# Optimization experiments

Measured on AMD Instinct MI355X. Metric: run time of the kernel, lower is better.

The kernel has to match this reference:

```python
import jax, jax.numpy as jnp
import numpy as np

EPS = 1e-7
MAX_TAN_NORM = 10.0  # safe_expmap0 clamp


def logmap0(x):
    # x: [..., D] Lorentz point, x[..., 0] = time component (>= 1)
    x0 = x[..., :1]
    xs = x[..., 1:]
    d = jnp.arccosh(jnp.clip(x0, 1.0 + EPS, None))          # geodesic distance to origin
    ns = jnp.clip(jnp.linalg.norm(xs, axis=-1, keepdims=True), EPS, None)
    return jnp.concatenate([jnp.zeros_like(x0), d * xs / ns], axis=-1)


def safe_expmap0(u):
    # u: tangent at origin; time component is projected out (proju at origin)
    us = u[..., 1:]
    n = jnp.clip(jnp.linalg.norm(us, axis=-1, keepdims=True), EPS, None)
    nc = jnp.minimum(n, MAX_TAN_NORM)                        # clamp norm for stability
    usc = us * (nc / n)
    return jnp.concatenate([jnp.cosh(nc), jnp.sinh(nc) * usc / nc], axis=-1)


def projx(x):
    # re-project onto the hyperboloid: x0 = sqrt(1 + ||xs||^2)
    xs = x[..., 1:]
    x0 = jnp.sqrt(1.0 + jnp.sum(xs * xs, axis=-1, keepdims=True))
    return jnp.concatenate([x0, xs], axis=-1)


def lorentz_linear(x_hyp, W, b):
    t = logmap0(x_hyp)
    y = t @ W.T + b
    return projx(safe_expmap0(y))


def setup_inputs() -> dict:
    key = jax.random.key(0)
    ks = jax.random.split(key, 8)
    N, D_IN, D_HID, D_OUT = 8192, 1024, 4096, 1024
    s = 0.02
    x_sp = jax.random.normal(ks[0], (N, D_IN), dtype=jnp.float32)
    x_hyp = projx(x_sp)  # valid Lorentz point (time comp overwritten)
    W1 = jax.random.normal(ks[1], (D_HID, D_IN), dtype=jnp.float32) * s
    b1 = jnp.zeros((D_HID,), dtype=jnp.float32)
    W2 = jax.random.normal(ks[2], (D_HID, D_HID), dtype=jnp.float32) * s
    b2 = jnp.zeros((D_HID,), dtype=jnp.float32)
    W3 = jax.random.normal(ks[3], (D_OUT, D_HID), dtype=jnp.float32) * s
    b3 = jnp.zeros((D_OUT,), dtype=jnp.float32)
    return {"x_hyp": x_hyp, "W1": W1, "b1": b1, "W2": W2, "b2": b2, "W3": W3, "b3": b3}


def reference(x_hyp, W1, b1, W2, b2, W3, b3):
    # layers[:-1] with inter-layer logmap0 -> (dropout=identity in eval) -> expmap0 -> projx
    h = lorentz_linear(x_hyp, W1, b1)
    h = projx(safe_expmap0(logmap0(h)))
    h = lorentz_linear(h, W2, b2)
    h = projx(safe_expmap0(logmap0(h)))
    return lorentz_linear(h, W3, b3)
```

## Files before the change

kernel.cpp:

```cpp
#include <hip/hip_runtime.h>
#include <stdint.h>

#define EPSF 1e-7f
#define MAXTAN 10.0f

typedef __bf16 bf16x8 __attribute__((ext_vector_type(8)));
typedef float floatx4 __attribute__((ext_vector_type(4)));
typedef __attribute__((address_space(3))) void lds_void_t;
typedef __attribute__((address_space(1))) void gbl_void_t;

__device__ __forceinline__ unsigned short f2bf(float x) {
  union { float f; uint32_t u; } v; v.f = x;
  uint32_t u = v.u;
  u += 0x7fffu + ((u >> 16) & 1u);
  return (unsigned short)(u >> 16);
}
__device__ __forceinline__ float bf2f(unsigned short h) {
  union { uint32_t u; float f; } v; v.u = ((uint32_t)h) << 16;
  return v.f;
}

__global__ void k_sniff(const unsigned short* __restrict__ x, int* __restrict__ mode) {
  if (threadIdx.x == 0 && blockIdx.x == 0) {
    int sane = 0;
    for (int i = 0; i < 128; ++i) {
      unsigned short h = x[i];
      int e = (h >> 7) & 0xFF;
      if ((h & 0x7FFF) == 0 || (e >= 96 && e <= 140)) ++sane;
    }
    *mode = (sane >= 120) ? 1 : 0;
  }
}

__global__ void k_prep(const void* __restrict__ xv, unsigned short* __restrict__ xb,
                       float* __restrict__ sc0, float* __restrict__ x0c,
                       const int* __restrict__ mode) {
  const int row = blockIdx.x;
  const int tid = threadIdx.x;
  float4 v;
  if (*mode) {
    ushort4 u = ((const ushort4*)((const unsigned short*)xv + (size_t)row * 1024))[tid];
    v.x = bf2f(u.x); v.y = bf2f(u.y); v.z = bf2f(u.z); v.w = bf2f(u.w);
  } else {
    v = ((const float4*)((const float*)xv + (size_t)row * 1024))[tid];
  }
  ushort4 o;
  o.x = f2bf(v.x); o.y = f2bf(v.y); o.z = f2bf(v.z); o.w = f2bf(v.w);
  ((ushort4*)(xb + (size_t)row * 1024))[tid] = o;

  float s = v.x * v.x + v.y * v.y + v.z * v.z + v.w * v.w;
  if (tid == 0) s -= v.x * v.x;
  for (int off = 32; off; off >>= 1) s += __shfl_down(s, off, 64);
  __shared__ float red[4];
  if ((tid & 63) == 0) red[tid >> 6] = s;
  __syncthreads();
  if (tid == 0) {
    s = red[0] + red[1] + red[2] + red[3];
    float ns = fmaxf(sqrtf(s), EPSF);
    float d = acoshf(fmaxf(v.x, 1.0f + EPSF));
    sc0[row] = d / ns;
    x0c[row] = bf2f(o.x);
  }
}

template<int K8>
__global__ void k_cvtw(const void* __restrict__ in, unsigned short* __restrict__ out,
                       const int* __restrict__ mode, int n8, float* __restrict__ c0) {
  int i = blockIdx.x * 256 + threadIdx.x;
  if (i >= n8) return;
  if (*mode) {
    uint4 g = ((const uint4*)in)[i];
    ((uint4*)out)[i] = g;
    if (i % K8 == 0) c0[i / K8] = bf2f((unsigned short)(g.x & 0xFFFFu));
  } else {
    float4 a = ((const float4*)in)[2 * i];
    float4 b = ((const float4*)in)[2 * i + 1];
    ushort4 oa, ob;
    oa.x = f2bf(a.x); oa.y = f2bf(a.y); oa.z = f2bf(a.z); oa.w = f2bf(a.w);
    ob.x = f2bf(b.x); ob.y = f2bf(b.y); ob.z = f2bf(b.z); ob.w = f2bf(b.w);
    ((ushort4*)out)[2 * i] = oa;
    ((ushort4*)out)[2 * i + 1] = ob;
    if (i % K8 == 0) c0[i / K8] = bf2f(oa.x);
  }
}

__global__ void k_cvtb(const void* __restrict__ b1, const void* __restrict__ b2,
                       const void* __restrict__ b3, float* __restrict__ o1,
                       float* __restrict__ o2, float* __restrict__ o3,
                       const int* __restrict__ mode) {
  int i = blockIdx.x * 256 + threadIdx.x;
  int m = *mode;
  if (i < 4096) o1[i] = m ? bf2f(((const unsigned short*)b1)[i]) : ((const float*)b1)[i];
  if (i < 4096) o2[i] = m ? bf2f(((const unsigned short*)b2)[i]) : ((const float*)b2)[i];
  if (i < 1024) o3[i] = m ? bf2f(((const unsigned short*)b3)[i]) : ((const float*)b3)[i];
}

template<int NBLK>
__global__ void k_sc(const float* __restrict__ part, const unsigned short* __restrict__ y,
                     int stride, float* __restrict__ sc, float* __restrict__ c0,
                     float* __restrict__ ssout, int nrows) {
  int i = blockIdx.x * 256 + threadIdx.x;
  if (i >= nrows) return;
  float s = 0.f;
#pragma unroll
  for (int j = 0; j < NBLK; ++j) s += part[(size_t)i * NBLK + j];
  float n = fmaxf(sqrtf(fmaxf(s, 0.f)), EPSF);
  sc[i] = fminf(n, MAXTAN) / n;
  c0[i] = bf2f(y[(size_t)i * stride]);
  if (ssout) ssout[i] = s;
}

__global__ void k_final(const unsigned short* __restrict__ y, const float* __restrict__ ss,
                        void* __restrict__ outv, const int* __restrict__ mode) {
  const int row = blockIdx.x;
  const int tid = threadIdx.x;
  float n = fmaxf(sqrtf(fmaxf(ss[row], 0.f)), EPSF);
  float nc = fminf(n, MAXTAN);
  float a = sinhf(nc) / n;
  ushort4 u = ((const ushort4*)(y + (size_t)row * 1024))[tid];
  float4 o;
  o.x = bf2f(u.x) * a; o.y = bf2f(u.y) * a;
  o.z = bf2f(u.z) * a; o.w = bf2f(u.w) * a;
  if (tid == 0) o.x = coshf(nc);
  if (*mode) {
    ushort4 o16;
    o16.x = f2bf(o.x); o16.y = f2bf(o.y); o16.z = f2bf(o.z); o16.w = f2bf(o.w);
    ((ushort4*)outv)[(size_t)row * 256 + tid] = o16;
  } else {
    ((float4*)outv)[(size_t)row * 256 + tid] = o;
  }
}

template<int N, int K, int NBLK>
__global__ __launch_bounds__(256) void k_gemm_bt(
    const unsigned short* __restrict__ A,
    const unsigned short* __restrict__ B,
    const float* __restrict__ bias,
    const float* __restrict__ sc,
    const float* __restrict__ c0f,
    const float* __restrict__ wc0,
    unsigned short* __restrict__ Cb,
    float* __restrict__ part)
{
  __shared__ __align__(16) unsigned short As[128 * 32];
  __shared__ __align__(16) unsigned short Bs[128 * 32];

  const int tid  = threadIdx.x;
  const int wave = tid >> 6;
  const int lane = tid & 63;
  const int quad = lane >> 4;
  const int m16  = lane & 15;

  const int bm = blockIdx.y * 128;
  const int bn = blockIdx.x * 128;

  const int srow = lane >> 2;
  const int scol = (((lane & 3) ^ ((srow >> 1) & 3)) << 3);

  const int wm = (wave >> 1) << 6;
  const int wn = (wave & 1) << 6;

  const int rsw = ((quad ^ ((m16 >> 1) & 3)) << 3);

  floatx4 acc[4][4];
#pragma unroll
  for (int i = 0; i < 4; ++i)
#pragma unroll
    for (int j = 0; j < 4; ++j)
#pragma unroll
      for (int r = 0; r < 4; ++r) acc[i][j][r] = 0.0f;

  for (int k0 = 0; k0 < K; k0 += 32) {
#pragma unroll
    for (int i = 0; i < 2; ++i) {
      const int c = wave * 2 + i;
      const unsigned short* ga = A + (size_t)(bm + c * 16 + srow) * K + k0 + scol;
      const unsigned short* gb = B + (size_t)(bn + c * 16 + srow) * K + k0 + scol;
      __builtin_amdgcn_global_load_lds((gbl_void_t*)(void*)ga,
                                       (lds_void_t*)(As + c * 512), 16, 0, 0);
      __builtin_amdgcn_global_load_lds((gbl_void_t*)(void*)gb,
                                       (lds_void_t*)(Bs + c * 512), 16, 0, 0);
    }
    __syncthreads();

    bf16x8 af[4], bfg[4];
#pragma unroll
    for (int t = 0; t < 4; ++t) {
      af[t]  = *(const bf16x8*)(As + (wm + t * 16 + m16) * 32 + rsw);
      bfg[t] = *(const bf16x8*)(Bs + (wn + t * 16 + m16) * 32 + rsw);
    }
#pragma unroll
    for (int mt = 0; mt < 4; ++mt)
#pragma unroll
      for (int nt = 0; nt < 4; ++nt)
        acc[mt][nt] = __builtin_amdgcn_mfma_f32_16x16x32_bf16(af[mt], bfg[nt], acc[mt][nt], 0, 0, 0);
    __syncthreads();
  }

#pragma unroll
  for (int mt = 0; mt < 4; ++mt) {
#pragma unroll
    for (int r = 0; r < 4; ++r) {
      const int gm = bm + wm + mt * 16 + quad * 4 + r;
      const float scv = sc[gm];
      const float c0v = c0f[gm];
      float sq = 0.f;
#pragma unroll
      for (int nt = 0; nt < 4; ++nt) {
        const int gn = bn + wn + nt * 16 + m16;
        float v = scv * (acc[mt][nt][r] - c0v * wc0[gn]) + bias[gn];
        Cb[(size_t)gm * N + gn] = f2bf(v);
        sq += (gn == 0) ? 0.f : v * v;
      }
      sq += __shfl_xor(sq, 1, 64);
      sq += __shfl_xor(sq, 2, 64);
      sq += __shfl_xor(sq, 4, 64);
      sq += __shfl_xor(sq, 8, 64);
      if (m16 == 0) part[(size_t)gm * NBLK + 2 * blockIdx.x + (wave & 1)] = sq;
    }
  }
}

extern "C" void kernel_launch(void* const* d_in, const int* in_sizes, int n_in,
                              void* d_out, int out_size, void* d_ws, size_t ws_size,
                              hipStream_t stream) {
  const void* x  = d_in[0];
  const void* W1 = d_in[1];
  const void* b1 = d_in[2];
  const void* W2 = d_in[3];
  const void* b2 = d_in[4];
  const void* W3 = d_in[5];
  const void* b3 = d_in[6];

  const int NR = 8192, DIN = 1024, DH = 4096, DOUT = 1024;

  char* ws = (char*)d_ws;
  size_t off = 0;
  int* mode = (int*)(ws + off);                        off += 256;
  unsigned short* W1b = (unsigned short*)(ws + off);   off += (size_t)DH * DIN * 2;
  unsigned short* W2b = (unsigned short*)(ws + off);   off += (size_t)DH * DH * 2;
  unsigned short* W3b = (unsigned short*)(ws + off);   off += (size_t)DOUT * DH * 2;
  unsigned short* xb  = (unsigned short*)(ws + off);   off += (size_t)NR * DIN * 2;
  unsigned short* y1  = (unsigned short*)(ws + off);   off += (size_t)NR * DH * 2;
  unsigned short* y2  = (unsigned short*)(ws + off);   off += (size_t)NR * DH * 2;
  unsigned short* y3  = (unsigned short*)(ws + off);   off += (size_t)NR * DOUT * 2;
  float* part1 = (float*)(ws + off);                   off += (size_t)NR * 64 * 4;
  float* part2 = (float*)(ws + off);                   off += (size_t)NR * 64 * 4;
  float* part3 = (float*)(ws + off);                   off += (size_t)NR * 16 * 4;
  float* sc0  = (float*)(ws + off);                    off += (size_t)NR * 4;
  float* x0c  = (float*)(ws + off);                    off += (size_t)NR * 4;
  float* sc1  = (float*)(ws + off);                    off += (size_t)NR * 4;
  float* c01  = (float*)(ws + off);                    off += (size_t)NR * 4;
  float* sc2  = (float*)(ws + off);                    off += (size_t)NR * 4;
  float* c02  = (float*)(ws + off);                    off += (size_t)NR * 4;
  float* ss3  = (float*)(ws + off);                    off += (size_t)NR * 4;
  float* w1c0 = (float*)(ws + off);                    off += (size_t)DH * 4;
  float* w2c0 = (float*)(ws + off);                    off += (size_t)DH * 4;
  float* w3c0 = (float*)(ws + off);                    off += (size_t)DOUT * 4;
  float* b1f  = (float*)(ws + off);                    off += (size_t)DH * 4;
  float* b2f  = (float*)(ws + off);                    off += (size_t)DH * 4;
  float* b3f  = (float*)(ws + off);                    off += (size_t)DOUT * 4;

  k_sniff<<<1, 64, 0, stream>>>((const unsigned short*)x, mode);

  k_cvtb<<<16, 256, 0, stream>>>(b1, b2, b3, b1f, b2f, b3f, mode);
  k_cvtw<128><<<(DH * DIN / 8 + 255) / 256, 256, 0, stream>>>(W1, W1b, mode, DH * DIN / 8, w1c0);
  k_cvtw<512><<<(DH * DH  / 8 + 255) / 256, 256, 0, stream>>>(W2, W2b, mode, DH * DH / 8, w2c0);
  k_cvtw<512><<<(DOUT * DH / 8 + 255) / 256, 256, 0, stream>>>(W3, W3b, mode, DOUT * DH / 8, w3c0);

  k_prep<<<NR, 256, 0, stream>>>(x, xb, sc0, x0c, mode);

  k_gemm_bt<4096, 1024, 64><<<dim3(DH / 128, NR / 128), 256, 0, stream>>>(
      xb, W1b, b1f, sc0, x0c, w1c0, y1, part1);
  k_sc<64><<<(NR + 255) / 256, 256, 0, stream>>>(part1, y1, DH, sc1, c01, nullptr, NR);

  k_gemm_bt<4096, 4096, 64><<<dim3(DH / 128, NR / 128), 256, 0, stream>>>(
      y1, W2b, b2f, sc1, c01, w2c0, y2, part2);
  k_sc<64><<<(NR + 255) / 256, 256, 0, stream>>>(part2, y2, DH, sc2, c02, nullptr, NR);

  k_gemm_bt<1024, 4096, 16><<<dim3(DOUT / 128, NR / 128), 256, 0, stream>>>(
      y2, W3b, b3f, sc2, c02, w3c0, y3, part3);
  k_sc<16><<<(NR + 255) / 256, 256, 0, stream>>>(part3, y3, DOUT, sc0, x0c, ss3, NR);

  k_final<<<NR, 256, 0, stream>>>(y3, ss3, d_out, mode);
}
```

Baseline: 713.9 us.

## Remap GEMM block indices for XCD-aware L2 locality and fuse init kernels

Replaces the 2D grid of the three bf16 GEMMs with a 1D grid whose block index is remapped, so the blocks on each of the 8 XCDs cover a compact sub-rectangle of the output. This is meant to improve L2 reuse of the A and B tiles. It also sets launch_bounds to 4 blocks per SM and precomputes the global load pointers, advancing them by 32 each k-step instead of recomputing addresses. The mode sniff and bias conversion are merged into one kernel to save a launch. The mapping hardcodes the grid shapes and assumes round-robin dispatch of blocks across XCDs.

After: 674.2 us. 1.06x faster.

```diff
diff --git a/kernel.cpp b/kernel.cpp
--- a/kernel.cpp
+++ b/kernel.cpp
@@ -20,16 +20,32 @@
   return v.f;
 }
 
-__global__ void k_sniff(const unsigned short* __restrict__ x, int* __restrict__ mode) {
-  if (threadIdx.x == 0 && blockIdx.x == 0) {
-    int sane = 0;
-    for (int i = 0; i < 128; ++i) {
-      unsigned short h = x[i];
-      int e = (h >> 7) & 0xFF;
-      if ((h & 0x7FFF) == 0 || (e >= 96 && e <= 140)) ++sane;
-    }
-    *mode = (sane >= 120) ? 1 : 0;
-  }
+__device__ __forceinline__ int sniff_mode(const unsigned short* x) {
+  int sane = 0;
+  for (int i = 0; i < 128; ++i) {
+    unsigned short h = x[i];
+    int e = (h >> 7) & 0xFF;
+    if ((h & 0x7FFF) == 0 || (e >= 96 && e <= 140)) ++sane;
+  }
+  return (sane >= 120) ? 1 : 0;
+}
+
+__global__ void k_init(const unsigned short* __restrict__ x, int* __restrict__ modeg,
+                       const void* __restrict__ b1, const void* __restrict__ b2,
+                       const void* __restrict__ b3, float* __restrict__ o1,
+                       float* __restrict__ o2, float* __restrict__ o3) {
+  __shared__ int mds;
+  if (threadIdx.x == 0) {
+    int m = sniff_mode(x);
+    mds = m;
+    if (blockIdx.x == 0) *modeg = m;
+  }
+  __syncthreads();
+  int m = mds;
+  int i = blockIdx.x * 256 + threadIdx.x;
+  if (i < 4096) o1[i] = m ? bf2f(((const unsigned short*)b1)[i]) : ((const float*)b1)[i];
+  if (i < 4096) o2[i] = m ? bf2f(((const unsigned short*)b2)[i]) : ((const float*)b2)[i];
+  if (i < 1024) o3[i] = m ? bf2f(((const unsigned short*)b3)[i]) : ((const float*)b3)[i];
 }
 
 __global__ void k_prep(const void* __restrict__ xv, unsigned short* __restrict__ xb,
@@ -84,17 +100,6 @@
   }
 }
 
-__global__ void k_cvtb(const void* __restrict__ b1, const void* __restrict__ b2,
-                       const void* __restrict__ b3, float* __restrict__ o1,
-                       float* __restrict__ o2, float* __restrict__ o3,
-                       const int* __restrict__ mode) {
-  int i = blockIdx.x * 256 + threadIdx.x;
-  int m = *mode;
-  if (i < 4096) o1[i] = m ? bf2f(((const unsigned short*)b1)[i]) : ((const float*)b1)[i];
-  if (i < 4096) o2[i] = m ? bf2f(((const unsigned short*)b2)[i]) : ((const float*)b2)[i];
-  if (i < 1024) o3[i] = m ? bf2f(((const unsigned short*)b3)[i]) : ((const float*)b3)[i];
-}
-
 template<int NBLK>
 __global__ void k_sc(const float* __restrict__ part, const unsigned short* __restrict__ y,
                      int stride, float* __restrict__ sc, float* __restrict__ c0,
@@ -131,8 +136,8 @@
   }
 }
 
-template<int N, int K, int NBLK>
-__global__ __launch_bounds__(256) void k_gemm_bt(
+template<int N, int K, int NBLK, int GX>
+__global__ __launch_bounds__(256, 4) void k_gemm_bt(
     const unsigned short* __restrict__ A,
     const unsigned short* __restrict__ B,
     const float* __restrict__ bias,
@@ -151,8 +156,18 @@
   const int quad = lane >> 4;
   const int m16  = lane & 15;
 
-  const int bm = blockIdx.y * 128;
-  const int bn = blockIdx.x * 128;
+  const int j = blockIdx.x & 7;
+  const int k = blockIdx.x >> 3;
+  int bxi, byi;
+  if (GX == 32) {
+    bxi = 16 * (j & 1) + (k & 15);
+    byi = 16 * (j >> 1) + (k >> 4);
+  } else {
+    bxi = k & 7;
+    byi = 8 * j + (k >> 3);
+  }
+  const int bm = byi * 128;
+  const int bn = bxi * 128;
 
   const int srow = lane >> 2;
   const int scol = (((lane & 3) ^ ((srow >> 1) & 3)) << 3);
@@ -162,25 +177,30 @@
 
   const int rsw = ((quad ^ ((m16 >> 1) & 3)) << 3);
 
+  const int c0i = wave * 2;
+  const unsigned short* ga0 = A + (size_t)(bm + c0i * 16 + srow) * K + scol;
+  const unsigned short* ga1 = ga0 + (size_t)16 * K;
+  const unsigned short* gb0 = B + (size_t)(bn + c0i * 16 + srow) * K + scol;
+  const unsigned short* gb1 = gb0 + (size_t)16 * K;
+
   floatx4 acc[4][4];
 #pragma unroll
   for (int i = 0; i < 4; ++i)
 #pragma unroll
-    for (int j = 0; j < 4; ++j)
-#pragma unroll
-      for (int r = 0; r < 4; ++r) acc[i][j][r] = 0.0f;
+    for (int jj = 0; jj < 4; ++jj)
+#pragma unroll
+      for (int r = 0; r < 4; ++r) acc[i][jj][r] = 0.0f;
 
   for (int k0 = 0; k0 < K; k0 += 32) {
-#pragma unroll
-    for (int i = 0; i < 2; ++i) {
-      const int c = wave * 2 + i;
-      const unsigned short* ga = A + (size_t)(bm + c * 16 + srow) * K + k0 + scol;
-      const unsigned short* gb = B + (size_t)(bn + c * 16 + srow) * K + k0 + scol;
-      __builtin_amdgcn_global_load_lds((gbl_void_t*)(void*)ga,
-                                       (lds_void_t*)(As + c * 512), 16, 0, 0);
-      __builtin_amdgcn_global_load_lds((gbl_void_t*)(void*)gb,
-                                       (lds_void_t*)(Bs + c * 512), 16, 0, 0);
-    }
+    __builtin_amdgcn_global_load_lds((gbl_void_t*)(void*)ga0,
+                                     (lds_void_t*)(As + c0i * 512), 16, 0, 0);
+    __builtin_amdgcn_global_load_lds((gbl_void_t*)(void*)ga1,
+                                     (lds_void_t*)(As + c0i * 512 + 512), 16, 0, 0);
+    __builtin_amdgcn_global_load_lds((gbl_void_t*)(void*)gb0,
+                                     (lds_void_t*)(Bs + c0i * 512), 16, 0, 0);
+    __builtin_amdgcn_global_load_lds((gbl_void_t*)(void*)gb1,
+                                     (lds_void_t*)(Bs + c0i * 512 + 512), 16, 0, 0);
+    ga0 += 32; ga1 += 32; gb0 += 32; gb1 += 32;
     __syncthreads();
 
     bf16x8 af[4], bfg[4];
@@ -216,7 +236,7 @@
       sq += __shfl_xor(sq, 2, 64);
       sq += __shfl_xor(sq, 4, 64);
       sq += __shfl_xor(sq, 8, 64);
-      if (m16 == 0) part[(size_t)gm * NBLK + 2 * blockIdx.x + (wave & 1)] = sq;
+      if (m16 == 0) part[(size_t)gm * NBLK + 2 * bxi + (wave & 1)] = sq;
     }
   }
 }
@@ -261,24 +281,23 @@
   float* b2f  = (float*)(ws + off);                    off += (size_t)DH * 4;
   float* b3f  = (float*)(ws + off);                    off += (size_t)DOUT * 4;
 
-  k_sniff<<<1, 64, 0, stream>>>((const unsigned short*)x, mode);
-
-  k_cvtb<<<16, 256, 0, stream>>>(b1, b2, b3, b1f, b2f, b3f, mode);
+  k_init<<<16, 256, 0, stream>>>((const unsigned short*)x, mode, b1, b2, b3, b1f, b2f, b3f);
+
   k_cvtw<128><<<(DH * DIN / 8 + 255) / 256, 256, 0, stream>>>(W1, W1b, mode, DH * DIN / 8, w1c0);
   k_cvtw<512><<<(DH * DH  / 8 + 255) / 256, 256, 0, stream>>>(W2, W2b, mode, DH * DH / 8, w2c0);
   k_cvtw<512><<<(DOUT * DH / 8 + 255) / 256, 256, 0, stream>>>(W3, W3b, mode, DOUT * DH / 8, w3c0);
 
   k_prep<<<NR, 256, 0, stream>>>(x, xb, sc0, x0c, mode);
 
-  k_gemm_bt<4096, 1024, 64><<<dim3(DH / 128, NR / 128), 256, 0, stream>>>(
+  k_gemm_bt<4096, 1024, 64, 32><<<2048, 256, 0, stream>>>(
       xb, W1b, b1f, sc0, x0c, w1c0, y1, part1);
   k_sc<64><<<(NR + 255) / 256, 256, 0, stream>>>(part1, y1, DH, sc1, c01, nullptr, NR);
 
-  k_gemm_bt<4096, 4096, 64><<<dim3(DH / 128, NR / 128), 256, 0, stream>>>(
+  k_gemm_bt<4096, 4096, 64, 32><<<2048, 256, 0, stream>>>(
       y1, W2b, b2f, sc1, c01, w2c0, y2, part2);
   k_sc<64><<<(NR + 255) / 256, 256, 0, stream>>>(part2, y2, DH, sc2, c02, nullptr, NR);
 
-  k_gemm_bt<1024, 4096, 16><<<dim3(DOUT / 128, NR / 128), 256, 0, stream>>>(
+  k_gemm_bt<1024, 4096, 16, 8><<<512, 256, 0, stream>>>(
       y2, W3b, b3f, sc2, c02, w3c0, y3, part3);
   k_sc<16><<<(NR + 255) / 256, 256, 0, stream>>>(part3, y3, DOUT, sc0, x0c, ss3, NR);
 
```
